# Optimization experiments

Hardware: AMD Instinct MI355X
Metric: run time of the kernel (lower is better)

The kernel has to match this reference:

```python
import jax, jax.numpy as jnp
import numpy as np

N = 100000      # nodes
MUL_IN = 256    # multiplicity of 0e and 1o in irreps_in ('256x0e + 256x1o')
MUL_H = 64      # multiplicity in MLP_irreps ('64x0e + 64x1o')
# irreps_nonlin = (64+64)x0e (scalars + gates) + 64x1o (gated)


def setup_inputs() -> dict:
    key = jax.random.key(0)
    k0, k1, k2, k3, k4 = jax.random.split(key, 5)
    # e3nn flat layout: [scalars (256), vectors (256*3, as (mul,3) flattened)]
    x = jax.random.normal(k0, (N, MUL_IN * 4), dtype=jnp.float32)
    # linear_1 block weights (e3nn Linear: randn init, output scaled by 1/sqrt(fan_in))
    w1_s = jax.random.normal(k1, (MUL_IN, 2 * MUL_H), dtype=jnp.float32)  # 0e->0e (scalars+gates)
    w1_v = jax.random.normal(k2, (MUL_IN, MUL_H), dtype=jnp.float32)      # 1o->1o
    # linear_2 block weights: 64x0e->1x0e, 64x1o->1x1o
    w2_s = jax.random.normal(k3, (MUL_H, 1), dtype=jnp.float32)
    w2_v = jax.random.normal(k4, (MUL_H, 1), dtype=jnp.float32)
    return {"x": x, "w1_s": w1_s, "w1_v": w1_v, "w2_s": w2_s, "w2_v": w2_v}


def reference(x, w1_s, w1_v, w2_s, w2_v):
    # ---- split input into irrep blocks ----
    xs = x[:, :MUL_IN]                          # [N, 256] 0e scalars
    xv = x[:, MUL_IN:].reshape(-1, MUL_IN, 3)   # [N, 256, 3] 1o vectors

    inv_in = np.float32(1.0 / np.sqrt(MUL_IN))
    # ---- linear_1: per-irrep block-diagonal matmuls (weight shared over m) ----
    h_s = (xs @ w1_s) * inv_in                              # [N, 128] scalars+gates
    h_v = jnp.einsum('nmi,mk->nki', xv, w1_v) * inv_in       # [N, 64, 3]

    # ---- Gate: act(scalars), act(gates) * gated_vectors ----
    scalars = h_s[:, :MUL_H]
    gates = h_s[:, MUL_H:]
    g_s = jax.nn.silu(scalars)                               # [N, 64]
    g_v = jax.nn.silu(gates)[:, :, None] * h_v               # [N, 64, 3]

    inv_h = np.float32(1.0 / np.sqrt(MUL_H))
    # ---- linear_2: 64x0e -> 1x0e, 64x1o -> 1x1o ----
    out_s = (g_s @ w2_s) * inv_h                             # [N, 1]
    out_v = jnp.einsum('nmi,mk->nki', g_v, w2_v).reshape(-1, 3) * inv_h  # [N, 3]
    return jnp.concatenate([out_s, out_v], axis=1)           # [N, 4] = 1x0e + 1x1o
```

## Files before the change

kernel.cpp:

```cpp
#include <hip/hip_runtime.h>
#include <hip/hip_bf16.h>
#include <math.h>

#define N_ROWS  100000
#define NT_ROW  6250

typedef __attribute__((ext_vector_type(8))) short bf16x8;
typedef __attribute__((ext_vector_type(4))) float f32x4;

__device__ __forceinline__ float silu_f(float v) {
    return v * (1.0f / (1.0f + __expf(-v)));
}
__device__ __forceinline__ short f2bf(float f) {
    union { __hip_bfloat16 h; short s; } u;
    u.h = __float2bfloat16(f);
    return u.s;
}
__device__ __forceinline__ void stage16(const float* g, float* l) {
    __builtin_amdgcn_global_load_lds(
        (const __attribute__((address_space(1))) unsigned int*)g,
        (__attribute__((address_space(3))) unsigned int*)l,
        16, 0, 0);
}

__global__ __launch_bounds__(64)
void prep_wT(const float* __restrict__ w1_s, const float* __restrict__ w1_v,
             unsigned short* __restrict__ wTf)
{
    const int tp = blockIdx.x;
    const int t = tp >> 3, p = tp & 7;
    const int lane = threadIdx.x;
    const int l15 = lane & 15, lq = lane >> 4;
    const float* src  = (t < 8) ? w1_s : w1_v;
    const int    strd = (t < 8) ? 128 : 64;
    const int    scol = (t < 8) ? (t * 16 + l15) : (((t - 8) & 3) * 16 + l15);
    const int    k0   = 32 * p + 8 * lq;
    unsigned short o[8];
    #pragma unroll
    for (int e = 0; e < 8; ++e)
        o[e] = (unsigned short)f2bf(src[(k0 + e) * strd + scol]);
    *(ushort4*)(wTf + (size_t)tp * 512 + lane * 8)     = make_ushort4(o[0], o[1], o[2], o[3]);
    *(ushort4*)(wTf + (size_t)tp * 512 + lane * 8 + 4) = make_ushort4(o[4], o[5], o[6], o[7]);
}

__global__ __launch_bounds__(256, 4)
void ndr_mfma_kernel(const float* __restrict__ x,
                     const unsigned short* __restrict__ wTf,
                     const float* __restrict__ w2_s,
                     const float* __restrict__ w2_v,
                     float* __restrict__ out)
{
    __shared__ float  lds[2][16][128];
    __shared__ float4 red[4][16];

    const int lane = threadIdx.x & 63;
    const int wid  = threadIdx.x >> 6;
    const int l15  = lane & 15, lq = lane >> 4;
    const long long n0 = (long long)blockIdx.x * 16;

    const float w2sv = w2_s[16 * wid + l15];
    const float w2vv = w2_v[16 * wid + l15];

    const int sub = lane >> 5, slot = lane & 31;
    const float* sp[2];
    int sstep[2];
    #pragma unroll
    for (int jj = 0; jj < 2; ++jj) {
        const int j   = 2 * wid + jj;
        const int row = 2 * j + sub;
        const int g   = slot ^ (row & 7);
        const int isxs = (g < 8);
        sstep[jj] = isxs ? 32 : 96;
        sp[jj] = x + (n0 + row) * 1024 + (isxs ? 4 * g : 256 + 4 * (g - 8));
    }

    f32x4 acc[5];
    #pragma unroll
    for (int t = 0; t < 5; ++t) acc[t] = (f32x4){0.f, 0.f, 0.f, 0.f};

    const char* wbase = (const char*)wTf + lane * 16;

    #pragma unroll
    for (int jj = 0; jj < 2; ++jj)
        stage16(sp[jj],            &lds[0][0][0] + (2 * wid + jj) * 256);
    #pragma unroll
    for (int jj = 0; jj < 2; ++jj)
        stage16(sp[jj] + sstep[jj], &lds[1][0][0] + (2 * wid + jj) * 256);

    const int r7 = l15 & 7;

    #pragma unroll 1
    for (int p = 0; p < 8; ++p) {
        asm volatile("s_waitcnt vmcnt(2)" ::: "memory");
        __builtin_amdgcn_s_barrier();

        const float* rb = &lds[p & 1][l15][0];
        float4 s0 = *(const float4*)(rb + 4 * ((2 * lq    ) ^ r7));
        float4 s1 = *(const float4*)(rb + 4 * ((2 * lq + 1) ^ r7));
        float4 v0 = *(const float4*)(rb + 4 * ((8 + 6 * lq + 0) ^ r7));
        float4 v1 = *(const float4*)(rb + 4 * ((8 + 6 * lq + 1) ^ r7));
        float4 v2 = *(const float4*)(rb + 4 * ((8 + 6 * lq + 2) ^ r7));
        float4 v3 = *(const float4*)(rb + 4 * ((8 + 6 * lq + 3) ^ r7));
        float4 v4 = *(const float4*)(rb + 4 * ((8 + 6 * lq + 4) ^ r7));
        float4 v5 = *(const float4*)(rb + 4 * ((8 + 6 * lq + 5) ^ r7));

        const float xs[8]  = {s0.x, s0.y, s0.z, s0.w, s1.x, s1.y, s1.z, s1.w};
        const float xv[24] = {v0.x, v0.y, v0.z, v0.w, v1.x, v1.y, v1.z, v1.w,
                              v2.x, v2.y, v2.z, v2.w, v3.x, v3.y, v3.z, v3.w,
                              v4.x, v4.y, v4.z, v4.w, v5.x, v5.y, v5.z, v5.w};
        bf16x8 a_s, a_v0, a_v1, a_v2;
        #pragma unroll
        for (int e = 0; e < 8; ++e) {
            a_s[e]  = f2bf(xs[e]);
            a_v0[e] = f2bf(xv[3 * e + 0]);
            a_v1[e] = f2bf(xv[3 * e + 1]);
            a_v2[e] = f2bf(xv[3 * e + 2]);
        }

        bf16x8 bf[5];
        #pragma unroll
        for (int t = 0; t < 5; ++t)
            bf[t] = *(const bf16x8*)(wbase + (size_t)(wid + 4 * t) * 8192
                                           + (size_t)p * 1024);

        asm volatile("s_waitcnt lgkmcnt(0)" ::: "memory");
        __builtin_amdgcn_s_barrier();

        if (p + 2 < 8) {
            #pragma unroll
            for (int jj = 0; jj < 2; ++jj)
                stage16(sp[jj] + (p + 2) * sstep[jj],
                        &lds[p & 1][0][0] + (2 * wid + jj) * 256);
        }

        acc[0] = __builtin_amdgcn_mfma_f32_16x16x32_bf16(a_s,  bf[0], acc[0], 0, 0, 0);
        acc[1] = __builtin_amdgcn_mfma_f32_16x16x32_bf16(a_s,  bf[1], acc[1], 0, 0, 0);
        acc[2] = __builtin_amdgcn_mfma_f32_16x16x32_bf16(a_v0, bf[2], acc[2], 0, 0, 0);
        acc[3] = __builtin_amdgcn_mfma_f32_16x16x32_bf16(a_v1, bf[3], acc[3], 0, 0, 0);
        acc[4] = __builtin_amdgcn_mfma_f32_16x16x32_bf16(a_v2, bf[4], acc[4], 0, 0, 0);
    }

    const float inv_in = 0.0625f, inv_h = 0.125f;
    #pragma unroll
    for (int j = 0; j < 4; ++j) {
        float hs = acc[0][j] * inv_in;
        float hg = acc[1][j] * inv_in;
        float gg = silu_f(hg);
        float ps  = silu_f(hs) * w2sv;
        float pv0 = gg * (acc[2][j] * inv_in) * w2vv;
        float pv1 = gg * (acc[3][j] * inv_in) * w2vv;
        float pv2 = gg * (acc[4][j] * inv_in) * w2vv;
        #pragma unroll
        for (int off = 1; off <= 8; off <<= 1) {
            ps  += __shfl_xor(ps,  off, 64);
            pv0 += __shfl_xor(pv0, off, 64);
            pv1 += __shfl_xor(pv1, off, 64);
            pv2 += __shfl_xor(pv2, off, 64);
        }
        if (l15 == 0)
            red[wid][lq * 4 + j] = make_float4(ps, pv0, pv1, pv2);
    }
    __syncthreads();
    if (wid == 0 && lane < 16) {
        float4 a = red[0][lane], b = red[1][lane],
               c = red[2][lane], d = red[3][lane];
        float4 o = make_float4((a.x + b.x + c.x + d.x) * inv_h,
                               (a.y + b.y + c.y + d.y) * inv_h,
                               (a.z + b.z + c.z + d.z) * inv_h,
                               (a.w + b.w + c.w + d.w) * inv_h);
        *(float4*)(out + (n0 + lane) * 4) = o;
    }
}

extern "C" void kernel_launch(void* const* d_in, const int* in_sizes, int n_in,
                              void* d_out, int out_size, void* d_ws, size_t ws_size,
                              hipStream_t stream) {
    const float* x    = (const float*)d_in[0];
    const float* w1_s = (const float*)d_in[1];
    const float* w1_v = (const float*)d_in[2];
    const float* w2_s = (const float*)d_in[3];
    const float* w2_v = (const float*)d_in[4];
    float* out = (float*)d_out;
    unsigned short* wTf = (unsigned short*)d_ws;

    prep_wT<<<160, 64, 0, stream>>>(w1_s, w1_v, wTf);
    ndr_mfma_kernel<<<NT_ROW, 256, 0, stream>>>(x, wTf, w2_s, w2_v, out);
}
```

Baseline: 112.4 us.

## Make MFMA kernel persistent with whole-tile double-buffered LDS prefetch

Replaces the one-block-per-16-row-tile launch with a persistent grid of 256 blocks that loop over tiles. Each block stages a full 16x1024 fp32 tile (64KB) into LDS and prefetches the next tile into a second buffer while computing the current one. This is meant to remove per-block launch and prologue costs and the per-K-step barrier pair of the old 8-step pipeline. In exchange, occupancy drops to one 256-thread block per CU with 130KB of LDS, so memory latency is hidden by only four waves plus the prefetch depth.

Measured after the change: 189.1 us. +68.2%, slower.

```diff
diff --git a/kernel.cpp b/kernel.cpp
--- a/kernel.cpp
+++ b/kernel.cpp
@@ -4,6 +4,7 @@
 
 #define N_ROWS  100000
 #define NT_ROW  6250
+#define GRID    256
 
 typedef __attribute__((ext_vector_type(8))) short bf16x8;
 typedef __attribute__((ext_vector_type(4))) float f32x4;
@@ -43,133 +44,134 @@
     *(ushort4*)(wTf + (size_t)tp * 512 + lane * 8 + 4) = make_ushort4(o[4], o[5], o[6], o[7]);
 }
 
-__global__ __launch_bounds__(256, 4)
+__global__ __launch_bounds__(256, 1)
 void ndr_mfma_kernel(const float* __restrict__ x,
                      const unsigned short* __restrict__ wTf,
                      const float* __restrict__ w2_s,
                      const float* __restrict__ w2_v,
                      float* __restrict__ out)
 {
-    __shared__ float  lds[2][16][128];
-    __shared__ float4 red[4][16];
+    __shared__ float Lds[2 * 16384 + 512];
+    float4* red = (float4*)&Lds[32768];
 
     const int lane = threadIdx.x & 63;
     const int wid  = threadIdx.x >> 6;
-    const int l15  = lane & 15, lq = lane >> 4;
-    const long long n0 = (long long)blockIdx.x * 16;
+    const int l15  = lane & 15, lq = lane >> 4, r7 = l15 & 7;
 
     const float w2sv = w2_s[16 * wid + l15];
     const float w2vv = w2_v[16 * wid + l15];
-
-    const int sub = lane >> 5, slot = lane & 31;
-    const float* sp[2];
-    int sstep[2];
-    #pragma unroll
-    for (int jj = 0; jj < 2; ++jj) {
-        const int j   = 2 * wid + jj;
-        const int row = 2 * j + sub;
-        const int g   = slot ^ (row & 7);
-        const int isxs = (g < 8);
-        sstep[jj] = isxs ? 32 : 96;
-        sp[jj] = x + (n0 + row) * 1024 + (isxs ? 4 * g : 256 + 4 * (g - 8));
-    }
-
-    f32x4 acc[5];
-    #pragma unroll
-    for (int t = 0; t < 5; ++t) acc[t] = (f32x4){0.f, 0.f, 0.f, 0.f};
-
     const char* wbase = (const char*)wTf + lane * 16;
 
+    #define CHUNK(tb, j, bufb)                                              \
+        do {                                                                \
+            const int r_ = 4 * wid + ((j) >> 2);                            \
+            const int q_ = (j) & 3;                                         \
+            const int g_ = (q_ * 64 + lane) ^ (r_ & 7);                     \
+            stage16(x + (tb) + (long long)r_ * 1024 + g_ * 4,               \
+                    (bufb) + r_ * 1024 + q_ * 256);                         \
+        } while (0)
+
+    long long T = blockIdx.x;
     #pragma unroll
-    for (int jj = 0; jj < 2; ++jj)
-        stage16(sp[jj],            &lds[0][0][0] + (2 * wid + jj) * 256);
-    #pragma unroll
-    for (int jj = 0; jj < 2; ++jj)
-        stage16(sp[jj] + sstep[jj], &lds[1][0][0] + (2 * wid + jj) * 256);
+    for (int j = 0; j < 16; ++j) CHUNK(T * 16384, j, &Lds[0]);
 
-    const int r7 = l15 & 7;
+    int cur = 0, par = 0;
 
     #pragma unroll 1
-    for (int p = 0; p < 8; ++p) {
-        asm volatile("s_waitcnt vmcnt(2)" ::: "memory");
+    for (; T < NT_ROW; T += GRID) {
+        const long long Tn = T + GRID;
+        asm volatile("s_waitcnt vmcnt(0)" ::: "memory");
         __builtin_amdgcn_s_barrier();
 
-        const float* rb = &lds[p & 1][l15][0];
-        float4 s0 = *(const float4*)(rb + 4 * ((2 * lq    ) ^ r7));
-        float4 s1 = *(const float4*)(rb + 4 * ((2 * lq + 1) ^ r7));
-        float4 v0 = *(const float4*)(rb + 4 * ((8 + 6 * lq + 0) ^ r7));
-        float4 v1 = *(const float4*)(rb + 4 * ((8 + 6 * lq + 1) ^ r7));
-        float4 v2 = *(const float4*)(rb + 4 * ((8 + 6 * lq + 2) ^ r7));
-        float4 v3 = *(const float4*)(rb + 4 * ((8 + 6 * lq + 3) ^ r7));
-        float4 v4 = *(const float4*)(rb + 4 * ((8 + 6 * lq + 4) ^ r7));
-        float4 v5 = *(const float4*)(rb + 4 * ((8 + 6 * lq + 5) ^ r7));
+        f32x4 acc[5];
+        #pragma unroll
+        for (int t = 0; t < 5; ++t) acc[t] = (f32x4){0.f, 0.f, 0.f, 0.f};
 
-        const float xs[8]  = {s0.x, s0.y, s0.z, s0.w, s1.x, s1.y, s1.z, s1.w};
-        const float xv[24] = {v0.x, v0.y, v0.z, v0.w, v1.x, v1.y, v1.z, v1.w,
-                              v2.x, v2.y, v2.z, v2.w, v3.x, v3.y, v3.z, v3.w,
-                              v4.x, v4.y, v4.z, v4.w, v5.x, v5.y, v5.z, v5.w};
-        bf16x8 a_s, a_v0, a_v1, a_v2;
-        #pragma unroll
-        for (int e = 0; e < 8; ++e) {
-            a_s[e]  = f2bf(xs[e]);
-            a_v0[e] = f2bf(xv[3 * e + 0]);
-            a_v1[e] = f2bf(xv[3 * e + 1]);
-            a_v2[e] = f2bf(xv[3 * e + 2]);
+        const float* rb = &Lds[cur * 16384] + l15 * 1024;
+        float* nb = &Lds[(cur ^ 1) * 16384];
+
+        #pragma unroll 1
+        for (int p = 0; p < 8; ++p) {
+            bf16x8 bf[5];
+            #pragma unroll
+            for (int t = 0; t < 5; ++t)
+                bf[t] = *(const bf16x8*)(wbase + (size_t)(wid + 4 * t) * 8192
+                                               + (size_t)p * 1024);
+
+            if (Tn < NT_ROW) {
+                if (p < 5) {
+                    CHUNK(Tn * 16384, 3 * p,     nb);
+                    CHUNK(Tn * 16384, 3 * p + 1, nb);
+                    CHUNK(Tn * 16384, 3 * p + 2, nb);
+                } else if (p == 5) {
+                    CHUNK(Tn * 16384, 15, nb);
+                }
+            }
+
+            float4 s0 = *(const float4*)(rb + 4 * ((8 * p + 2 * lq    ) ^ r7));
+            float4 s1 = *(const float4*)(rb + 4 * ((8 * p + 2 * lq + 1) ^ r7));
+            float4 v0 = *(const float4*)(rb + 4 * ((64 + 24 * p + 6 * lq + 0) ^ r7));
+            float4 v1 = *(const float4*)(rb + 4 * ((64 + 24 * p + 6 * lq + 1) ^ r7));
+            float4 v2 = *(const float4*)(rb + 4 * ((64 + 24 * p + 6 * lq + 2) ^ r7));
+            float4 v3 = *(const float4*)(rb + 4 * ((64 + 24 * p + 6 * lq + 3) ^ r7));
+            float4 v4 = *(const float4*)(rb + 4 * ((64 + 24 * p + 6 * lq + 4) ^ r7));
+            float4 v5 = *(const float4*)(rb + 4 * ((64 + 24 * p + 6 * lq + 5) ^ r7));
+
+            const float xs[8]  = {s0.x, s0.y, s0.z, s0.w, s1.x, s1.y, s1.z, s1.w};
+            const float xv[24] = {v0.x, v0.y, v0.z, v0.w, v1.x, v1.y, v1.z, v1.w,
+                                  v2.x, v2.y, v2.z, v2.w, v3.x, v3.y, v3.z, v3.w,
+                                  v4.x, v4.y, v4.z, v4.w, v5.x, v5.y, v5.z, v5.w};
+            bf16x8 a_s, a_v0, a_v1, a_v2;
+            #pragma unroll
+            for (int e = 0; e < 8; ++e) {
+                a_s[e]  = f2bf(xs[e]);
+                a_v0[e] = f2bf(xv[3 * e + 0]);
+                a_v1[e] = f2bf(xv[3 * e + 1]);
+                a_v2[e] = f2bf(xv[3 * e + 2]);
+            }
+
+            acc[0] = __builtin_amdgcn_mfma_f32_16x16x32_bf16(a_s,  bf[0], acc[0], 0, 0, 0);
+            acc[1] = __builtin_amdgcn_mfma_f32_16x16x32_bf16(a_s,  bf[1], acc[1], 0, 0, 0);
+            acc[2] = __builtin_amdgcn_mfma_f32_16x16x32_bf16(a_v0, bf[2], acc[2], 0, 0, 0);
+            acc[3] = __builtin_amdgcn_mfma_f32_16x16x32_bf16(a_v1, bf[3], acc[3], 0, 0, 0);
+            acc[4] = __builtin_amdgcn_mfma_f32_16x16x32_bf16(a_v2, bf[4], acc[4], 0, 0, 0);
         }
 
-        bf16x8 bf[5];
+        const float inv_in = 0.0625f, inv_h = 0.125f;
+        float4* rp = red + par * 64;
         #pragma unroll
-        for (int t = 0; t < 5; ++t)
-            bf[t] = *(const bf16x8*)(wbase + (size_t)(wid + 4 * t) * 8192
-                                           + (size_t)p * 1024);
-
+        for (int j = 0; j < 4; ++j) {
+            float hs = acc[0][j] * inv_in;
+            float hg = acc[1][j] * inv_in;
+            float gg = silu_f(hg);
+            float ps  = silu_f(hs) * w2sv;
+            float pv0 = gg * (acc[2][j] * inv_in) * w2vv;
+            float pv1 = gg * (acc[3][j] * inv_in) * w2vv;
+            float pv2 = gg * (acc[4][j] * inv_in) * w2vv;
+            #pragma unroll
+            for (int off = 1; off <= 8; off <<= 1) {
+                ps  += __shfl_xor(ps,  off, 64);
+                pv0 += __shfl_xor(pv0, off, 64);
+                pv1 += __shfl_xor(pv1, off, 64);
+                pv2 += __shfl_xor(pv2, off, 64);
+            }
+            if (l15 == 0)
+                rp[wid * 16 + lq * 4 + j] = make_float4(ps, pv0, pv1, pv2);
+        }
         asm volatile("s_waitcnt lgkmcnt(0)" ::: "memory");
         __builtin_amdgcn_s_barrier();
-
-        if (p + 2 < 8) {
-            #pragma unroll
-            for (int jj = 0; jj < 2; ++jj)
-                stage16(sp[jj] + (p + 2) * sstep[jj],
-                        &lds[p & 1][0][0] + (2 * wid + jj) * 256);
+        if (wid == 0 && lane < 16) {
+            float4 a = rp[lane], b = rp[16 + lane],
+                   c = rp[32 + lane], d = rp[48 + lane];
+            *(float4*)(out + (T * 16 + lane) * 4) =
+                make_float4((a.x + b.x + c.x + d.x) * inv_h,
+                            (a.y + b.y + c.y + d.y) * inv_h,
+                            (a.z + b.z + c.z + d.z) * inv_h,
+                            (a.w + b.w + c.w + d.w) * inv_h);
         }
-
-        acc[0] = __builtin_amdgcn_mfma_f32_16x16x32_bf16(a_s,  bf[0], acc[0], 0, 0, 0);
-        acc[1] = __builtin_amdgcn_mfma_f32_16x16x32_bf16(a_s,  bf[1], acc[1], 0, 0, 0);
-        acc[2] = __builtin_amdgcn_mfma_f32_16x16x32_bf16(a_v0, bf[2], acc[2], 0, 0, 0);
-        acc[3] = __builtin_amdgcn_mfma_f32_16x16x32_bf16(a_v1, bf[3], acc[3], 0, 0, 0);
-        acc[4] = __builtin_amdgcn_mfma_f32_16x16x32_bf16(a_v2, bf[4], acc[4], 0, 0, 0);
+        cur ^= 1; par ^= 1;
     }
-
-    const float inv_in = 0.0625f, inv_h = 0.125f;
-    #pragma unroll
-    for (int j = 0; j < 4; ++j) {
-        float hs = acc[0][j] * inv_in;
-        float hg = acc[1][j] * inv_in;
-        float gg = silu_f(hg);
-        float ps  = silu_f(hs) * w2sv;
-        float pv0 = gg * (acc[2][j] * inv_in) * w2vv;
-        float pv1 = gg * (acc[3][j] * inv_in) * w2vv;
-        float pv2 = gg * (acc[4][j] * inv_in) * w2vv;
-        #pragma unroll
-        for (int off = 1; off <= 8; off <<= 1) {
-            ps  += __shfl_xor(ps,  off, 64);
-            pv0 += __shfl_xor(pv0, off, 64);
-            pv1 += __shfl_xor(pv1, off, 64);
-            pv2 += __shfl_xor(pv2, off, 64);
-        }
-        if (l15 == 0)
-            red[wid][lq * 4 + j] = make_float4(ps, pv0, pv1, pv2);
-    }
-    __syncthreads();
-    if (wid == 0 && lane < 16) {
-        float4 a = red[0][lane], b = red[1][lane],
-               c = red[2][lane], d = red[3][lane];
-        float4 o = make_float4((a.x + b.x + c.x + d.x) * inv_h,
-                               (a.y + b.y + c.y + d.y) * inv_h,
-                               (a.z + b.z + c.z + d.z) * inv_h,
-                               (a.w + b.w + c.w + d.w) * inv_h);
-        *(float4*)(out + (n0 + lane) * 4) = o;
-    }
+    #undef CHUNK
 }
 
 extern "C" void kernel_launch(void* const* d_in, const int* in_sizes, int n_in,
@@ -184,5 +186,5 @@
     unsigned short* wTf = (unsigned short*)d_ws;
 
     prep_wT<<<160, 64, 0, stream>>>(w1_s, w1_v, wTf);
-    ndr_mfma_kernel<<<NT_ROW, 256, 0, stream>>>(x, wTf, w2_s, w2_v, out);
+    ndr_mfma_kernel<<<GRID, 256, 0, stream>>>(x, wTf, w2_s, w2_v, out);
 }
```
